# Kernel tuning notes

Measured on AMD Instinct MI355X. Metric: run time of the kernel, lower is better.

The kernel has to match this reference:

```python
import math
import jax, jax.numpy as jnp
import numpy as np

_EPS = 1e-6
N_DELTA, N_THETA, N_GAMMA = 4, 8, 16
N_OSC = N_DELTA + N_THETA + N_GAMMA  # 28
N_STEPS = 5
DT = 0.01
MATCH_THRESHOLD = 0.3
TWO_PI = 2.0 * math.pi

# Band natural frequencies (Hz): delta ~2, theta ~6, gamma ~40 (surrogate for DiscreteDeltaThetaGamma)
_OMEGA = TWO_PI * jnp.concatenate([
    jnp.full((N_DELTA,), 2.0, jnp.float32),
    jnp.full((N_THETA,), 6.0, jnp.float32),
    jnp.full((N_GAMMA,), 40.0, jnp.float32),
])


def setup_inputs() -> dict:
    key = jax.random.key(0)
    ks = jax.random.split(key, 12)
    N, D, H = 4096, 128, 64
    s1 = 1.0 / math.sqrt(D)
    s2 = 1.0 / math.sqrt(H)
    return {
        "detections_t": jax.random.normal(ks[0], (N, D), jnp.float32),
        "detections_t1": jax.random.normal(ks[1], (N, D), jnp.float32),
        # phase MLP
        "Wp1": jax.random.normal(ks[2], (D, H), jnp.float32) * s1,
        "bp1": jnp.zeros((H,), jnp.float32),
        "Wp2": jax.random.normal(ks[3], (H, N_OSC), jnp.float32) * s2,
        "bp2": jnp.zeros((N_OSC,), jnp.float32),
        # amplitude MLP
        "Wa1": jax.random.normal(ks[4], (D, H), jnp.float32) * s1,
        "ba1": jnp.zeros((H,), jnp.float32),
        "Wa2": jax.random.normal(ks[5], (H, N_OSC), jnp.float32) * s2,
        "ba2": jnp.zeros((N_OSC,), jnp.float32),
    }


def _encode(x, W1, b1, W2, b2, Wa1, ba1, Wa2, ba2):
    h = jax.nn.relu(x @ W1 + b1)
    phase = jnp.mod(h @ W2 + b2, TWO_PI)          # (N, n_osc)
    ha = jax.nn.relu(x @ Wa1 + ba1)
    amp = jax.nn.softplus(ha @ Wa2 + ba2)          # (N, n_osc)
    return phase, amp


def _evolve(phase, amp):
    # Kuramoto-style mean-field dynamics (surrogate for DiscreteDeltaThetaGamma.integrate)
    def step(carry, _):
        ph, am = carry
        c, s = jnp.cos(ph), jnp.sin(ph)
        mc = jnp.mean(c, axis=-1, keepdims=True)
        ms = jnp.mean(s, axis=-1, keepdims=True)
        # R*sin(psi - phi) = ms*cos(phi) - mc*sin(phi)
        coupling = ms * c - mc * s
        ph = jnp.mod(ph + DT * (_OMEGA + am * coupling), TWO_PI)
        return (ph, am), None
    (phase, amp), _ = jax.lax.scan(step, (phase, amp), None, length=N_STEPS)
    return phase, amp


def _phase_similarity(pa, pb):
    # sum_k cos(pa_k - pb_k) / (sqrt(K)+eps)^2, via real matmuls (no [Na,Nb,K] tensor)
    ca, sa = jnp.cos(pa), jnp.sin(pa)
    cb, sb = jnp.cos(pb), jnp.sin(pb)
    denom = (math.sqrt(N_OSC) + _EPS) ** 2
    return (ca @ cb.T + sa @ sb.T) / denom


def _greedy_match(sim, threshold):
    N_t, N_t1 = sim.shape
    max_sims = jnp.max(sim, axis=1)
    max_idxs = jnp.argmax(sim, axis=1)
    order = jnp.argsort(-max_sims)  # descending

    def step(used, idx):
        j = max_idxs[idx]
        ok = (~used[j]) & (max_sims[idx] > threshold)
        used = used.at[j].set(used[j] | ok)
        return used, jnp.where(ok, j, -1)

    used0 = jnp.zeros((N_t1,), bool)
    _, match_vals = jax.lax.scan(step, used0, order)
    matches = jnp.full((N_t,), -1, jnp.int32).at[order].set(match_vals.astype(jnp.int32))
    return matches


def reference(detections_t, detections_t1, Wp1, bp1, Wp2, bp2, Wa1, ba1, Wa2, ba2):
    phase_t, amp_t = _encode(detections_t, Wp1, bp1, Wp2, bp2, Wa1, ba1, Wa2, ba2)
    phase_t1, _ = _encode(detections_t1, Wp1, bp1, Wp2, bp2, Wa1, ba1, Wa2, ba2)
    phase_t_ev, _ = _evolve(phase_t, amp_t)
    sim = _phase_similarity(phase_t_ev, phase_t1)
    matches = _greedy_match(sim, MATCH_THRESHOLD)
    return matches, sim
```

## Files before the change

kernel.cpp:

```cpp
#include <hip/hip_runtime.h>
#include <math.h>

#define NDET 4096
#define DIM  128
#define HID  64
#define NOSC 28
#define KPAD 64

constexpr float TWO_PI_F = 6.28318530717958647692f;

typedef _Float16 f16x8 __attribute__((ext_vector_type(8)));
typedef float    f32x4 __attribute__((ext_vector_type(4)));

__device__ __forceinline__ unsigned f2sort(float f){
    unsigned u = __float_as_uint(f);
    return (u & 0x80000000u) ? ~u : (u | 0x80000000u);
}
__device__ __forceinline__ float sort2f(unsigned u){
    return __uint_as_float((u & 0x80000000u) ? (u & 0x7fffffffu) : ~u);
}
__device__ __forceinline__ float lane_bcast(float v, int t){
    return __uint_as_float(__builtin_amdgcn_readlane(__float_as_uint(v), t));
}

__global__ __launch_bounds__(256) void encode_kernel(
    const float* __restrict__ det_t, const float* __restrict__ det_t1,
    const float* __restrict__ Wp1, const float* __restrict__ bp1,
    const float* __restrict__ Wp2, const float* __restrict__ bp2,
    const float* __restrict__ Wa1, const float* __restrict__ ba1,
    const float* __restrict__ Wa2, const float* __restrict__ ba2,
    _Float16* __restrict__ Ahi, _Float16* __restrict__ Alo,
    _Float16* __restrict__ Bhi, _Float16* __restrict__ Blo)
{
    const int tid  = threadIdx.x;
    const int lane = tid & 63;
    const int wv   = tid >> 6;
    const int b    = blockIdx.x;
    const bool isT = b < 512;
    const int lr = __builtin_amdgcn_readfirstlane(((b & 511) << 3) + wv * 2);
    const float* __restrict__ src = (isT ? det_t : det_t1) + (size_t)lr * DIM;

    float h0 = bp1[lane], h1 = h0;
    float g0 = 0.0f, g1 = 0.0f;
    if (isT){
        g0 = ba1[lane]; g1 = g0;
        #pragma unroll 8
        for (int d = 0; d < DIM; ++d){
            float x0 = src[d], x1 = src[DIM + d];
            float wp = Wp1[d * HID + lane];
            float wa = Wa1[d * HID + lane];
            h0 = fmaf(x0, wp, h0);  h1 = fmaf(x1, wp, h1);
            g0 = fmaf(x0, wa, g0);  g1 = fmaf(x1, wa, g1);
        }
        g0 = fmaxf(g0, 0.0f); g1 = fmaxf(g1, 0.0f);
    } else {
        #pragma unroll 8
        for (int d = 0; d < DIM; ++d){
            float x0 = src[d], x1 = src[DIM + d];
            float wp = Wp1[d * HID + lane];
            h0 = fmaf(x0, wp, h0);  h1 = fmaf(x1, wp, h1);
        }
    }
    h0 = fmaxf(h0, 0.0f); h1 = fmaxf(h1, 0.0f);

    const int k  = lane & 31;
    const bool kv = k < NOSC;
    const int kc = kv ? k : 0;

    float pa = bp2[kc], pb = pa;
    #pragma unroll 16
    for (int t = 0; t < HID; ++t){
        float w2 = Wp2[t * NOSC + kc];
        pa = fmaf(lane_bcast(h0, t), w2, pa);
        pb = fmaf(lane_bcast(h1, t), w2, pb);
    }
    float aa = 0.0f, ab = 0.0f;
    if (isT){
        aa = ba2[kc]; ab = aa;
        #pragma unroll 16
        for (int t = 0; t < HID; ++t){
            float w2 = Wa2[t * NOSC + kc];
            aa = fmaf(lane_bcast(g0, t), w2, aa);
            ab = fmaf(lane_bcast(g1, t), w2, ab);
        }
    }

    const bool hiHalf = lane >= 32;
    float p2 = hiHalf ? pb : pa;
    float ph = fmodf(p2, TWO_PI_F);
    if (ph < 0.0f) ph += TWO_PI_F;

    if (isT){
        float a2 = hiHalf ? ab : aa;
        float am = fmaxf(a2, 0.0f) + log1pf(expf(-fabsf(a2)));
        const float omega = TWO_PI_F * ((k < 4) ? 2.0f : (k < 12) ? 6.0f : 40.0f);
        for (int s5 = 0; s5 < 5; ++s5){
            float sn, cs;
            sincosf(ph, &sn, &cs);
            float c = kv ? cs : 0.0f;
            float s = kv ? sn : 0.0f;
            float sc = c, ss = s;
            sc += __shfl_xor(sc, 16); ss += __shfl_xor(ss, 16);
            sc += __shfl_xor(sc,  8); ss += __shfl_xor(ss,  8);
            sc += __shfl_xor(sc,  4); ss += __shfl_xor(ss,  4);
            sc += __shfl_xor(sc,  2); ss += __shfl_xor(ss,  2);
            sc += __shfl_xor(sc,  1); ss += __shfl_xor(ss,  1);
            float mc = sc * (1.0f / NOSC);
            float ms = ss * (1.0f / NOSC);
            float coupling = ms * c - mc * s;
            ph += 0.01f * (omega + am * coupling);
            ph = fmodf(ph, TWO_PI_F);
            if (ph < 0.0f) ph += TWO_PI_F;
        }
    }

    const int row = lr + (hiHalf ? 1 : 0);
    _Float16* __restrict__ dhi = isT ? Ahi : Bhi;
    _Float16* __restrict__ dlo = isT ? Alo : Blo;
    const size_t rb = (size_t)row * KPAD;
    if (kv){
        float sn, cs;
        sincosf(ph, &sn, &cs);
        _Float16 ch = (_Float16)cs;
        _Float16 sh = (_Float16)sn;
        _Float16 cl = (_Float16)(cs - (float)ch);
        _Float16 sl = (_Float16)(sn - (float)sh);
        dhi[rb + k]        = ch;
        dhi[rb + NOSC + k] = sh;
        dlo[rb + k]        = cl;
        dlo[rb + NOSC + k] = sl;
    } else {
        const int kk = k - NOSC;
        dhi[rb + 56 + kk] = (_Float16)0.0f;
        dhi[rb + 60 + kk] = (_Float16)0.0f;
        dlo[rb + 56 + kk] = (_Float16)0.0f;
        dlo[rb + 60 + kk] = (_Float16)0.0f;
    }
}

__global__ __launch_bounds__(256) void sim_kernel(
    const _Float16* __restrict__ Ahi, const _Float16* __restrict__ Alo,
    const _Float16* __restrict__ Bhi, const _Float16* __restrict__ Blo,
    float* __restrict__ sim_out, unsigned long long* __restrict__ rowmax)
{
    const int tid  = threadIdx.x;
    const int lane = tid & 63;
    const int wid  = tid >> 6;
    const int i0 = blockIdx.y * 128 + (wid & 1) * 64;
    const int j0 = blockIdx.x * 128 + (wid >> 1) * 64;
    const int r16 = lane & 15;
    const int g   = lane >> 4;

    f16x8 ahi[4][2], alo[4][2];
    #pragma unroll
    for (int ib = 0; ib < 4; ++ib)
        #pragma unroll
        for (int kc = 0; kc < 2; ++kc){
            const size_t off = (size_t)(i0 + ib*16 + r16) * KPAD + kc*32 + g*8;
            ahi[ib][kc] = *(const f16x8*)&Ahi[off];
            alo[ib][kc] = *(const f16x8*)&Alo[off];
        }

    const float inv_denom =
        (float)(1.0 / ((5.2915026221291814 + 1e-6) * (5.2915026221291814 + 1e-6)));

    float bv[4] = {-3.4e38f, -3.4e38f, -3.4e38f, -3.4e38f};
    int   bj[4] = {0, 0, 0, 0};

    #pragma unroll 1
    for (int jb = 0; jb < 4; ++jb){
        f16x8 bhi[2], blo[2];
        #pragma unroll
        for (int kc = 0; kc < 2; ++kc){
            const size_t off = (size_t)(j0 + jb*16 + r16) * KPAD + kc*32 + g*8;
            bhi[kc] = *(const f16x8*)&Bhi[off];
            blo[kc] = *(const f16x8*)&Blo[off];
        }

        f32x4 acc[4] = {};
        #pragma unroll
        for (int ib = 0; ib < 4; ++ib){
            #pragma unroll
            for (int kc = 0; kc < 2; ++kc){
                acc[ib] = __builtin_amdgcn_mfma_f32_16x16x32_f16(bhi[kc], alo[ib][kc], acc[ib], 0, 0, 0);
                acc[ib] = __builtin_amdgcn_mfma_f32_16x16x32_f16(blo[kc], ahi[ib][kc], acc[ib], 0, 0, 0);
                acc[ib] = __builtin_amdgcn_mfma_f32_16x16x32_f16(bhi[kc], ahi[ib][kc], acc[ib], 0, 0, 0);
            }
        }

        #pragma unroll
        for (int ib = 0; ib < 4; ++ib){
            const int i = i0 + ib*16 + r16;
            f32x4 v = acc[ib];
            float4 out = make_float4(v[0]*inv_denom, v[1]*inv_denom,
                                     v[2]*inv_denom, v[3]*inv_denom);
            *(float4*)&sim_out[(size_t)i * NDET + j0 + jb*16 + g*4] = out;
            float vv[4] = {out.x, out.y, out.z, out.w};
            #pragma unroll
            for (int r = 0; r < 4; ++r){
                if (vv[r] > bv[ib]){ bv[ib] = vv[r]; bj[ib] = j0 + jb*16 + g*4 + r; }
            }
        }
    }

    #pragma unroll
    for (int ib = 0; ib < 4; ++ib){
        const int i = i0 + ib*16 + r16;
        unsigned long long key =
            ((unsigned long long)f2sort(bv[ib]) << 32) | (unsigned)(NDET - 1 - bj[ib]);
        unsigned long long o;
        o = __shfl_xor(key, 16); if (o > key) key = o;
        o = __shfl_xor(key, 32); if (o > key) key = o;
        if (g == 0) atomicMax(&rowmax[i], key);
    }
}

__global__ __launch_bounds__(1024) void match_kernel(
    const unsigned long long* __restrict__ rowmax,
    float* __restrict__ matches)
{
    __shared__ unsigned long long colwin[NDET];
    const int tid = threadIdx.x;

    #pragma unroll
    for (int t = 0; t < 4; ++t) colwin[tid + t*1024] = 0ull;
    __syncthreads();

    unsigned long long keys[4];
    #pragma unroll
    for (int t = 0; t < 4; ++t){
        const int i = tid + t*1024;
        unsigned long long key = rowmax[i];
        keys[t] = key;
        unsigned hi = (unsigned)(key >> 32);
        float v = sort2f(hi);
        if (v > 0.3f){
            int j = NDET - 1 - (int)(key & 0xffffffffu);
            unsigned long long ck =
                ((unsigned long long)hi << 32) | (unsigned)(NDET - 1 - i);
            atomicMax(&colwin[j], ck);
        }
    }
    __syncthreads();

    #pragma unroll
    for (int t = 0; t < 4; ++t){
        const int i = tid + t*1024;
        unsigned long long key = keys[t];
        unsigned hi = (unsigned)(key >> 32);
        float v = sort2f(hi);
        int j = NDET - 1 - (int)(key & 0xffffffffu);
        unsigned long long ck =
            ((unsigned long long)hi << 32) | (unsigned)(NDET - 1 - i);
        matches[i] = (v > 0.3f && colwin[j] == ck) ? (float)j : -1.0f;
    }
}

extern "C" void kernel_launch(void* const* d_in, const int* in_sizes, int n_in,
                              void* d_out, int out_size, void* d_ws, size_t ws_size,
                              hipStream_t stream)
{
    const float* det_t  = (const float*)d_in[0];
    const float* det_t1 = (const float*)d_in[1];
    const float* Wp1 = (const float*)d_in[2];
    const float* bp1 = (const float*)d_in[3];
    const float* Wp2 = (const float*)d_in[4];
    const float* bp2 = (const float*)d_in[5];
    const float* Wa1 = (const float*)d_in[6];
    const float* ba1 = (const float*)d_in[7];
    const float* Wa2 = (const float*)d_in[8];
    const float* ba2 = (const float*)d_in[9];

    float* out     = (float*)d_out;
    float* matches = out;
    float* sim     = out + NDET;

    char* ws = (char*)d_ws;
    unsigned long long* rowmax = (unsigned long long*)ws;
    _Float16* Ahi = (_Float16*)(ws + 32768);
    _Float16* Alo = Ahi + (size_t)NDET * KPAD;
    _Float16* Bhi = Alo + (size_t)NDET * KPAD;
    _Float16* Blo = Bhi + (size_t)NDET * KPAD;

    hipMemsetAsync(d_ws, 0, 32768, stream);

    encode_kernel<<<1024, 256, 0, stream>>>(
        det_t, det_t1, Wp1, bp1, Wp2, bp2, Wa1, ba1, Wa2, ba2, Ahi, Alo, Bhi, Blo);

    sim_kernel<<<dim3(NDET / 128, NDET / 128), 256, 0, stream>>>(
        Ahi, Alo, Bhi, Blo, sim, rowmax);

    match_kernel<<<1, 1024, 0, stream>>>(rowmax, matches);
}
```

Baseline: 128.1 us.

## Prefetch B tiles, pack encode stores, fold rowmax zeroing into encode

Result: no change. 128.8 us (+0.5%).

```diff
diff --git a/kernel.cpp b/kernel.cpp
--- a/kernel.cpp
+++ b/kernel.cpp
@@ -21,6 +21,11 @@
 }
 __device__ __forceinline__ float lane_bcast(float v, int t){
     return __uint_as_float(__builtin_amdgcn_readlane(__float_as_uint(v), t));
+}
+__device__ __forceinline__ unsigned packh(_Float16 a, _Float16 b){
+    union { _Float16 h; unsigned short u; } ua, ub;
+    ua.h = a; ub.h = b;
+    return (unsigned)ua.u | ((unsigned)ub.u << 16);
 }
 
 __global__ __launch_bounds__(256) void encode_kernel(
@@ -30,12 +35,17 @@
     const float* __restrict__ Wa1, const float* __restrict__ ba1,
     const float* __restrict__ Wa2, const float* __restrict__ ba2,
     _Float16* __restrict__ Ahi, _Float16* __restrict__ Alo,
-    _Float16* __restrict__ Bhi, _Float16* __restrict__ Blo)
+    _Float16* __restrict__ Bhi, _Float16* __restrict__ Blo,
+    unsigned long long* __restrict__ rowmax)
 {
     const int tid  = threadIdx.x;
     const int lane = tid & 63;
     const int wv   = tid >> 6;
     const int b    = blockIdx.x;
+
+    const int gtid = b * 256 + tid;
+    if (gtid < NDET) rowmax[gtid] = 0ull;
+
     const bool isT = b < 512;
     const int lr = __builtin_amdgcn_readfirstlane(((b & 511) << 3) + wv * 2);
     const float* __restrict__ src = (isT ? det_t : det_t1) + (size_t)lr * DIM;
@@ -115,9 +125,9 @@
     }
 
     const int row = lr + (hiHalf ? 1 : 0);
-    _Float16* __restrict__ dhi = isT ? Ahi : Bhi;
-    _Float16* __restrict__ dlo = isT ? Alo : Blo;
-    const size_t rb = (size_t)row * KPAD;
+    unsigned* __restrict__ dhi = (unsigned*)(isT ? Ahi : Bhi);
+    unsigned* __restrict__ dlo = (unsigned*)(isT ? Alo : Blo);
+    unsigned hw = 0u, lw = 0u;
     if (kv){
         float sn, cs;
         sincosf(ph, &sn, &cs);
@@ -125,17 +135,11 @@
         _Float16 sh = (_Float16)sn;
         _Float16 cl = (_Float16)(cs - (float)ch);
         _Float16 sl = (_Float16)(sn - (float)sh);
-        dhi[rb + k]        = ch;
-        dhi[rb + NOSC + k] = sh;
-        dlo[rb + k]        = cl;
-        dlo[rb + NOSC + k] = sl;
-    } else {
-        const int kk = k - NOSC;
-        dhi[rb + 56 + kk] = (_Float16)0.0f;
-        dhi[rb + 60 + kk] = (_Float16)0.0f;
-        dlo[rb + 56 + kk] = (_Float16)0.0f;
-        dlo[rb + 60 + kk] = (_Float16)0.0f;
-    }
+        hw = packh(ch, sh);
+        lw = packh(cl, sl);
+    }
+    dhi[row * (KPAD/2) + k] = hw;
+    dlo[row * (KPAD/2) + k] = lw;
 }
 
 __global__ __launch_bounds__(256) void sim_kernel(
@@ -167,14 +171,24 @@
     float bv[4] = {-3.4e38f, -3.4e38f, -3.4e38f, -3.4e38f};
     int   bj[4] = {0, 0, 0, 0};
 
-    #pragma unroll 1
+    f16x8 pbh[2][2], pbl[2][2];
+    #pragma unroll
+    for (int kc = 0; kc < 2; ++kc){
+        const size_t off = (size_t)(j0 + r16) * KPAD + kc*32 + g*8;
+        pbh[0][kc] = *(const f16x8*)&Bhi[off];
+        pbl[0][kc] = *(const f16x8*)&Blo[off];
+    }
+
+    #pragma unroll
     for (int jb = 0; jb < 4; ++jb){
-        f16x8 bhi[2], blo[2];
-        #pragma unroll
-        for (int kc = 0; kc < 2; ++kc){
-            const size_t off = (size_t)(j0 + jb*16 + r16) * KPAD + kc*32 + g*8;
-            bhi[kc] = *(const f16x8*)&Bhi[off];
-            blo[kc] = *(const f16x8*)&Blo[off];
+        const int cur = jb & 1, nxt = cur ^ 1;
+        if (jb < 3){
+            #pragma unroll
+            for (int kc = 0; kc < 2; ++kc){
+                const size_t off = (size_t)(j0 + (jb+1)*16 + r16) * KPAD + kc*32 + g*8;
+                pbh[nxt][kc] = *(const f16x8*)&Bhi[off];
+                pbl[nxt][kc] = *(const f16x8*)&Blo[off];
+            }
         }
 
         f32x4 acc[4] = {};
@@ -182,9 +196,9 @@
         for (int ib = 0; ib < 4; ++ib){
             #pragma unroll
             for (int kc = 0; kc < 2; ++kc){
-                acc[ib] = __builtin_amdgcn_mfma_f32_16x16x32_f16(bhi[kc], alo[ib][kc], acc[ib], 0, 0, 0);
-                acc[ib] = __builtin_amdgcn_mfma_f32_16x16x32_f16(blo[kc], ahi[ib][kc], acc[ib], 0, 0, 0);
-                acc[ib] = __builtin_amdgcn_mfma_f32_16x16x32_f16(bhi[kc], ahi[ib][kc], acc[ib], 0, 0, 0);
+                acc[ib] = __builtin_amdgcn_mfma_f32_16x16x32_f16(pbh[cur][kc], alo[ib][kc], acc[ib], 0, 0, 0);
+                acc[ib] = __builtin_amdgcn_mfma_f32_16x16x32_f16(pbl[cur][kc], ahi[ib][kc], acc[ib], 0, 0, 0);
+                acc[ib] = __builtin_amdgcn_mfma_f32_16x16x32_f16(pbh[cur][kc], ahi[ib][kc], acc[ib], 0, 0, 0);
             }
         }
 
@@ -282,10 +296,9 @@
     _Float16* Bhi = Alo + (size_t)NDET * KPAD;
     _Float16* Blo = Bhi + (size_t)NDET * KPAD;
 
-    hipMemsetAsync(d_ws, 0, 32768, stream);
-
     encode_kernel<<<1024, 256, 0, stream>>>(
-        det_t, det_t1, Wp1, bp1, Wp2, bp2, Wa1, ba1, Wa2, ba2, Ahi, Alo, Bhi, Blo);
+        det_t, det_t1, Wp1, bp1, Wp2, bp2, Wa1, ba1, Wa2, ba2,
+        Ahi, Alo, Bhi, Blo, rowmax);
 
     sim_kernel<<<dim3(NDET / 128, NDET / 128), 256, 0, stream>>>(
         Ahi, Alo, Bhi, Blo, sim, rowmax);
```
